# Performance work log

Measured on AMD Instinct MI355X. Metric: run time of the kernel, lower is better.

## Reference

```python
import jax, jax.numpy as jnp
import numpy as np

N_NODES = 1_000_000   # nodal points, 3 DOFs each
N_ELEMS = 500_000     # H8 (8-node hexahedral) elements
N_TYPES = 64          # distinct element stiffness matrices (24x24)


def setup_inputs() -> dict:
    key = jax.random.key(0)
    k1, k2, k3, k4 = jax.random.split(key, 4)
    U = jax.random.normal(k1, (N_NODES, 3), dtype=jnp.float32)
    filters = jax.random.normal(k2, (N_TYPES, 24, 24), dtype=jnp.float32)
    H8types = jax.random.randint(k3, (N_ELEMS,), 0, N_TYPES, dtype=jnp.int32)
    nodIdx = jax.random.randint(k4, (N_ELEMS, 8), 0, N_NODES, dtype=jnp.int32)
    return {"U": U, "filters": filters, "H8types": H8types, "nodIdx": nodIdx}


def reference(U, filters, H8types, nodIdx):
    """FEM stiffness matvec KU = sum_e scatter(K_type(e) @ gather(U, e)).

    U:       [N, 3]      nodal displacements (3 DOFs per node)
    filters: [T, 24, 24] per-type element stiffness matrices
    H8types: [E]         element type index into filters
    nodIdx:  [E, 8]      element -> node connectivity
    returns KU: [N, 3]
    """
    E = nodIdx.shape[0]
    # gather the 8 nodes x 3 DOFs of each element -> [E, 24]
    ue = U[nodIdx].reshape(E, 24)
    # per-type stiffness for each element -> [E, 24, 24]
    Ke = filters[H8types]
    # per-element force vector f_e = K_e @ u_e -> [E, 24]
    fe = jnp.einsum('eij,ej->ei', Ke, ue)
    # scatter-add element forces back to nodal DOFs
    KU = jnp.zeros_like(U).at[nodIdx.reshape(-1)].add(fe.reshape(E * 8, 3))
    return KU
```

## Files before the change

### kernel.cpp

```cpp
#include <hip/hip_runtime.h>


#define NTYPES    64
#define KSTRIDE   580
#define RSHIFT    11
#define RNODES    2048
#define MAXB      512
#define CAP       10240
#define K1_TPB    1024
#define K2_TPB    512
#define PREP_TPB  256

typedef int          nint4  __attribute__((ext_vector_type(4)));
typedef unsigned int nuint2 __attribute__((ext_vector_type(2)));

__device__ __forceinline__ unsigned bf16_rne(float f) {
    unsigned b = __float_as_uint(f);
    return (b + 0x7FFFu + ((b >> 16) & 1u)) >> 16;
}


__global__ __launch_bounds__(PREP_TPB) void pack_u_kernel(
    const float* __restrict__ U, nuint2* __restrict__ Ub, int n_nodes)
{
    int n = blockIdx.x * PREP_TPB + threadIdx.x;
    if (n >= n_nodes) return;
    const float* up = U + (size_t)n * 3;
    unsigned bx = bf16_rne(up[0]);
    unsigned by = bf16_rne(up[1]);
    unsigned bz = bf16_rne(up[2]);
    nuint2 v = { bx | (by << 16), bz };
    Ub[n] = v;
}


__global__ __launch_bounds__(K1_TPB, 1) void feconv_bin_kernel(
    const nuint2* __restrict__ Ub,
    const float* __restrict__ K,
    const int*   __restrict__ types,
    const int*   __restrict__ nodIdx,
    float*       __restrict__ KU,
    unsigned*    __restrict__ tails,
    unsigned*    __restrict__ recs,
    int n_elems, int n_buckets)
{
    extern __shared__ float sK[];
    __shared__ unsigned sCnt[MAXB];
    __shared__ unsigned sBase[MAXB];

    for (int w = threadIdx.x; w < NTYPES * 576; w += K1_TPB) {
        int t = w / 576;
        int r = w - t * 576;
        sK[t * KSTRIDE + r] = K[w];
    }
    for (int i = threadIdx.x; i < n_buckets; i += K1_TPB) sCnt[i] = 0;
    __syncthreads();

    const int e = blockIdx.x * K1_TPB + threadIdx.x;
    int nodes[8];
    int tt = -1;

    if (e < n_elems) {
        tt = __builtin_nontemporal_load(&types[e]);
        const nint4* q = (const nint4*)(nodIdx + (size_t)e * 8);
        nint4 a = __builtin_nontemporal_load(q);
        nint4 b = __builtin_nontemporal_load(q + 1);
        nodes[0] = a.x; nodes[1] = a.y; nodes[2] = a.z; nodes[3] = a.w;
        nodes[4] = b.x; nodes[5] = b.y; nodes[6] = b.z; nodes[7] = b.w;
#pragma unroll
        for (int j = 0; j < 8; ++j)
            atomicAdd(&sCnt[(unsigned)nodes[j] >> RSHIFT], 1u);
    }
    __syncthreads();

    for (int b = threadIdx.x; b < n_buckets; b += K1_TPB) {
        unsigned c = sCnt[b];
        sBase[b] = c ? atomicAdd(&tails[b], c) : 0u;
        sCnt[b] = 0;
    }
    __syncthreads();

    if (tt >= 0) {
        float ue[24];
#pragma unroll
        for (int j = 0; j < 8; ++j) {
            nuint2 v = Ub[nodes[j]];
            ue[3 * j + 0] = __uint_as_float(v.x << 16);
            ue[3 * j + 1] = __uint_as_float(v.x & 0xFFFF0000u);
            ue[3 * j + 2] = __uint_as_float(v.y << 16);
        }

        const float4* Kt4 = (const float4*)(sK + tt * KSTRIDE);
#pragma unroll
        for (int j = 0; j < 8; ++j) {
            float a0 = 0.f, a1 = 0.f, a2 = 0.f;
#pragma unroll
            for (int q = 0; q < 6; ++q) {
                float4 k0 = Kt4[(3 * j + 0) * 6 + q];
                float4 k1 = Kt4[(3 * j + 1) * 6 + q];
                float4 k2 = Kt4[(3 * j + 2) * 6 + q];
                float u0 = ue[4 * q + 0], u1 = ue[4 * q + 1];
                float u2 = ue[4 * q + 2], u3 = ue[4 * q + 3];
                a0 += k0.x * u0 + k0.y * u1 + k0.z * u2 + k0.w * u3;
                a1 += k1.x * u0 + k1.y * u1 + k1.z * u2 + k1.w * u3;
                a2 += k2.x * u0 + k2.y * u1 + k2.z * u2 + k2.w * u3;
            }
            unsigned n = (unsigned)nodes[j];
            unsigned b = n >> RSHIFT;
            unsigned pos = sBase[b] + atomicAdd(&sCnt[b], 1u);
            if (pos < CAP) {
                unsigned local = n & (RNODES - 1);
                size_t base = 3 * ((size_t)b * CAP + pos);
                recs[base + 0] = (__float_as_uint(a0) & ~15u) | (local & 15u);
                recs[base + 1] = (__float_as_uint(a1) & ~15u) | ((local >> 4) & 15u);
                recs[base + 2] = (__float_as_uint(a2) & ~15u) | (local >> 8);
            } else {
                atomicAdd(&KU[(size_t)n * 3 + 0], a0);
                atomicAdd(&KU[(size_t)n * 3 + 1], a1);
                atomicAdd(&KU[(size_t)n * 3 + 2], a2);
            }
        }
    }
}


__global__ __launch_bounds__(K2_TPB) void feconv_acc_kernel(
    const unsigned* __restrict__ recs,
    const unsigned* __restrict__ tails,
    float*          __restrict__ KU,
    int n_nodes)
{
    __shared__ float sAcc[RNODES * 3];
    const int b = blockIdx.x;

    for (int i = threadIdx.x; i < RNODES * 3; i += K2_TPB) sAcc[i] = 0.f;
    __syncthreads();

    unsigned cnt = tails[b];
    if (cnt > CAP) cnt = CAP;
    const unsigned* base = recs + 3 * ((size_t)b * CAP);
    for (unsigned i = threadIdx.x; i < cnt; i += K2_TPB) {
        unsigned w0 = base[3 * i + 0];
        unsigned w1 = base[3 * i + 1];
        unsigned w2 = base[3 * i + 2];
        unsigned local = (w0 & 15u) | ((w1 & 15u) << 4) | ((w2 & 7u) << 8);
        unsigned o = local * 3;
        atomicAdd(&sAcc[o + 0], __uint_as_float(w0 & ~15u));
        atomicAdd(&sAcc[o + 1], __uint_as_float(w1 & ~15u));
        atomicAdd(&sAcc[o + 2], __uint_as_float(w2 & ~15u));
    }
    __syncthreads();

    const int nbase = b * RNODES;
    int limit = n_nodes - nbase;
    if (limit > RNODES) limit = RNODES;
    limit *= 3;
    float* out = KU + (size_t)nbase * 3;
    for (int i = threadIdx.x; i < limit; i += K2_TPB) out[i] += sAcc[i];
}


__global__ __launch_bounds__(256) void feconv_elem_kernel(
    const float* __restrict__ U, const float* __restrict__ K,
    const int* __restrict__ types, const int* __restrict__ nodIdx,
    float* __restrict__ KU, int n_elems)
{
    int e = blockIdx.x * blockDim.x + threadIdx.x;
    if (e >= n_elems) return;
    int t = types[e];
    const int4* idx4 = (const int4*)(nodIdx + (size_t)e * 8);
    int4 iA = idx4[0], iB = idx4[1];
    int nodes[8] = {iA.x, iA.y, iA.z, iA.w, iB.x, iB.y, iB.z, iB.w};
    float ue[24];
#pragma unroll
    for (int j = 0; j < 8; ++j) {
        const float* up = U + (size_t)nodes[j] * 3;
        ue[3 * j + 0] = up[0]; ue[3 * j + 1] = up[1]; ue[3 * j + 2] = up[2];
    }
    const float* Kt = K + (size_t)t * 576;
#pragma unroll
    for (int i = 0; i < 24; ++i) {
        const float4* row = (const float4*)(Kt + i * 24);
        float acc = 0.f;
#pragma unroll
        for (int q = 0; q < 6; ++q) {
            float4 k = row[q];
            acc += k.x * ue[4 * q + 0] + k.y * ue[4 * q + 1]
                 + k.z * ue[4 * q + 2] + k.w * ue[4 * q + 3];
        }
        atomicAdd(&KU[(size_t)nodes[i / 3] * 3 + (i % 3)], acc);
    }
}

extern "C" void kernel_launch(void* const* d_in, const int* in_sizes, int n_in,
                              void* d_out, int out_size, void* d_ws, size_t ws_size,
                              hipStream_t stream) {
    const float* U      = (const float*)d_in[0];
    const float* Kf     = (const float*)d_in[1];
    const int*   types  = (const int*)d_in[2];
    const int*   nodIdx = (const int*)d_in[3];
    float*       KU     = (float*)d_out;

    const int n_elems = in_sizes[2];
    const int n_nodes = in_sizes[0] / 3;
    const int n_buckets = (n_nodes + RNODES - 1) / RNODES;

    (void)hipMemsetAsync(KU, 0, (size_t)out_size * sizeof(float), stream);

    const size_t ub_off  = 4096;
    const size_t rec_off = ub_off + (((size_t)n_nodes * 8 + 255) & ~255ull);
    const size_t need    = rec_off + (size_t)n_buckets * CAP * 12;

    if (n_buckets <= MAXB && ws_size >= need) {
        unsigned* tails = (unsigned*)d_ws;
        nuint2*   Ub    = (nuint2*)((char*)d_ws + ub_off);
        unsigned* recs  = (unsigned*)((char*)d_ws + rec_off);

        (void)hipMemsetAsync(tails, 0, 4096, stream);

        int gridP = (n_nodes + PREP_TPB - 1) / PREP_TPB;
        pack_u_kernel<<<gridP, PREP_TPB, 0, stream>>>(U, Ub, n_nodes);

        size_t lds_bytes = (size_t)NTYPES * KSTRIDE * sizeof(float);
        int grid1 = (n_elems + K1_TPB - 1) / K1_TPB;
        feconv_bin_kernel<<<grid1, K1_TPB, lds_bytes, stream>>>(
            Ub, Kf, types, nodIdx, KU, tails, recs, n_elems, n_buckets);
        feconv_acc_kernel<<<n_buckets, K2_TPB, 0, stream>>>(
            recs, tails, KU, n_nodes);
    } else {
        int block = 256;
        int grid = (n_elems + block - 1) / block;
        feconv_elem_kernel<<<grid, block, 0, stream>>>(
            U, Kf, types, nodIdx, KU, n_elems);
    }
}
```

Baseline: 237.9 us.

## Process two elements per thread and prefetch U gathers before bucket sync

```diff
diff --git a/kernel.cpp b/kernel.cpp
--- a/kernel.cpp
+++ b/kernel.cpp
@@ -8,6 +8,8 @@
 #define MAXB      512
 #define CAP       10240
 #define K1_TPB    1024
+#define K1_EPT    2
+#define K1_CHUNK  (K1_TPB * K1_EPT)
 #define K2_TPB    512
 #define PREP_TPB  256
 
@@ -34,7 +36,7 @@
 }
 
 
-__global__ __launch_bounds__(K1_TPB, 1) void feconv_bin_kernel(
+__global__ __launch_bounds__(K1_TPB, 4) void feconv_bin_kernel(
     const nuint2* __restrict__ Ub,
     const float* __restrict__ K,
     const int*   __restrict__ types,
@@ -56,20 +58,29 @@
     for (int i = threadIdx.x; i < n_buckets; i += K1_TPB) sCnt[i] = 0;
     __syncthreads();
 
-    const int e = blockIdx.x * K1_TPB + threadIdx.x;
-    int nodes[8];
-    int tt = -1;
-
-    if (e < n_elems) {
-        tt = __builtin_nontemporal_load(&types[e]);
-        const nint4* q = (const nint4*)(nodIdx + (size_t)e * 8);
-        nint4 a = __builtin_nontemporal_load(q);
-        nint4 b = __builtin_nontemporal_load(q + 1);
-        nodes[0] = a.x; nodes[1] = a.y; nodes[2] = a.z; nodes[3] = a.w;
-        nodes[4] = b.x; nodes[5] = b.y; nodes[6] = b.z; nodes[7] = b.w;
-#pragma unroll
-        for (int j = 0; j < 8; ++j)
-            atomicAdd(&sCnt[(unsigned)nodes[j] >> RSHIFT], 1u);
+    const int e0 = blockIdx.x * K1_CHUNK + threadIdx.x;
+    int     nodes[K1_EPT][8];
+    int     tt[K1_EPT];
+    nuint2  uu[K1_EPT][8];
+
+#pragma unroll
+    for (int k = 0; k < K1_EPT; ++k) {
+        int e = e0 + k * K1_TPB;
+        tt[k] = -1;
+        if (e < n_elems) {
+            tt[k] = __builtin_nontemporal_load(&types[e]);
+            const nint4* q = (const nint4*)(nodIdx + (size_t)e * 8);
+            nint4 a = __builtin_nontemporal_load(q);
+            nint4 b = __builtin_nontemporal_load(q + 1);
+            nodes[k][0] = a.x; nodes[k][1] = a.y; nodes[k][2] = a.z; nodes[k][3] = a.w;
+            nodes[k][4] = b.x; nodes[k][5] = b.y; nodes[k][6] = b.z; nodes[k][7] = b.w;
+#pragma unroll
+            for (int j = 0; j < 8; ++j)
+                uu[k][j] = Ub[nodes[k][j]];
+#pragma unroll
+            for (int j = 0; j < 8; ++j)
+                atomicAdd(&sCnt[(unsigned)nodes[k][j] >> RSHIFT], 1u);
+        }
     }
     __syncthreads();
 
@@ -80,17 +91,20 @@
     }
     __syncthreads();
 
-    if (tt >= 0) {
+#pragma unroll
+    for (int k = 0; k < K1_EPT; ++k) {
+        if (tt[k] < 0) continue;
+
         float ue[24];
 #pragma unroll
         for (int j = 0; j < 8; ++j) {
-            nuint2 v = Ub[nodes[j]];
+            nuint2 v = uu[k][j];
             ue[3 * j + 0] = __uint_as_float(v.x << 16);
             ue[3 * j + 1] = __uint_as_float(v.x & 0xFFFF0000u);
             ue[3 * j + 2] = __uint_as_float(v.y << 16);
         }
 
-        const float4* Kt4 = (const float4*)(sK + tt * KSTRIDE);
+        const float4* Kt4 = (const float4*)(sK + tt[k] * KSTRIDE);
 #pragma unroll
         for (int j = 0; j < 8; ++j) {
             float a0 = 0.f, a1 = 0.f, a2 = 0.f;
@@ -105,7 +119,7 @@
                 a1 += k1.x * u0 + k1.y * u1 + k1.z * u2 + k1.w * u3;
                 a2 += k2.x * u0 + k2.y * u1 + k2.z * u2 + k2.w * u3;
             }
-            unsigned n = (unsigned)nodes[j];
+            unsigned n = (unsigned)nodes[k][j];
             unsigned b = n >> RSHIFT;
             unsigned pos = sBase[b] + atomicAdd(&sCnt[b], 1u);
             if (pos < CAP) {
@@ -222,7 +236,7 @@
         pack_u_kernel<<<gridP, PREP_TPB, 0, stream>>>(U, Ub, n_nodes);
 
         size_t lds_bytes = (size_t)NTYPES * KSTRIDE * sizeof(float);
-        int grid1 = (n_elems + K1_TPB - 1) / K1_TPB;
+        int grid1 = (n_elems + K1_CHUNK - 1) / K1_CHUNK;
         feconv_bin_kernel<<<grid1, K1_TPB, lds_bytes, stream>>>(
             Ub, Kf, types, nodIdx, KU, tails, recs, n_elems, n_buckets);
         feconv_acc_kernel<<<n_buckets, K2_TPB, 0, stream>>>(
```

After: 216.4 us. 1.1x faster.
